# Kernel optimization log

Hardware: AMD Instinct MI355X
Metric: run time of the kernel (lower is better)

The kernel has to match this reference:

```python
import jax, jax.numpy as jnp
import numpy as np

N = 100000   # nodes
E = 800000   # edges
F_IN, H, C = 128, 128, 47
L = 3        # layers


def setup_inputs() -> dict:
    key = jax.random.key(0)
    ks = jax.random.split(key, 10)
    x = jax.random.normal(ks[0], (N, F_IN), dtype=jnp.float32)
    src = jax.random.randint(ks[1], (E,), 0, N, dtype=jnp.int32)
    dst = jax.random.randint(ks[2], (E,), 0, N, dtype=jnp.int32)
    w = jax.random.uniform(ks[3], (L, E), dtype=jnp.float32)
    W0 = jax.random.normal(ks[4], (F_IN, H), dtype=jnp.float32) * 0.05
    b0 = jnp.zeros((H,), jnp.float32)
    W1 = jax.random.normal(ks[5], (H, H), dtype=jnp.float32) * 0.05
    b1 = jnp.zeros((H,), jnp.float32)
    W2 = jax.random.normal(ks[6], (H, C), dtype=jnp.float32) * 0.05
    b2 = jnp.zeros((C,), jnp.float32)
    return {"x": x, "src": src, "dst": dst, "w": w,
            "W0": W0, "b0": b0, "W1": W1, "b1": b1, "W2": W2, "b2": b2}


def reference(x, src, dst, w, W0, b0, W1, b1, W2, b2):
    seg = lambda v, idx: jax.ops.segment_sum(v, idx, num_segments=N)
    ones = jnp.ones((src.shape[0],), x.dtype)
    # DGL GraphConv norm='both': structural degrees, clamped to >= 1
    inv_sqrt_out = jnp.maximum(seg(ones, src), 1.0) ** -0.5  # [N]
    inv_sqrt_in = jnp.maximum(seg(ones, dst), 1.0) ** -0.5   # [N]

    def gcn_layer(h, we, W, b):
        h = h * inv_sqrt_out[:, None]          # src normalization
        h = h @ W                               # linear (commutes with linear agg)
        m = h[src] * we[:, None]                # edge-weighted messages [E, d]
        agg = seg(m, dst)                       # scatter-add to dst [N, d]
        return agg * inv_sqrt_in[:, None] + b   # dst normalization + bias

    h = jax.nn.relu(gcn_layer(x, w[0], W0, b0))
    h = jax.nn.relu(gcn_layer(h, w[1], W1, b1))
    return gcn_layer(h, w[2], W2, b2)
```

## Files before the change

kernel.cpp:

```cpp
#include <hip/hip_runtime.h>


typedef short s16x8 __attribute__((ext_vector_type(8)));
typedef float f32x4 __attribute__((ext_vector_type(4)));

static constexpr int CAP = 24;

__device__ __forceinline__ unsigned short f2bf(float f) {
    unsigned int u = __float_as_uint(f);
    u += 0x7FFFu + ((u >> 16) & 1u);
    return (unsigned short)(u >> 16);
}
__device__ __forceinline__ float bf2f(unsigned short v) {
    return __uint_as_float((unsigned int)v << 16);
}

__global__ __launch_bounds__(256)
void fill_bucket(const int* __restrict__ src, const int* __restrict__ dst,
                 const float* __restrict__ w, int E,
                 int* __restrict__ dego, int* __restrict__ cursor,
                 float4* __restrict__ swb,
                 int* __restrict__ spill_cnt, int2* __restrict__ spill) {
    int e = blockIdx.x * blockDim.x + threadIdx.x;
    if (e >= E) return;
    int s = src[e];
    int d = dst[e];
    atomicAdd(&dego[s], 1);
    int pos = atomicAdd(&cursor[d], 1);
    if (pos < CAP) {
        swb[(size_t)d * CAP + pos] =
            make_float4(__int_as_float(s), w[e], w[E + e], w[2 * (size_t)E + e]);
    } else {
        int sp = atomicAdd(spill_cnt, 1);
        spill[sp] = make_int2(d, e);
    }
}

__global__ void invsqrt_kernel(const int* __restrict__ dego, const int* __restrict__ degi,
                               float* __restrict__ invo, float* __restrict__ invi, int N) {
    int i = blockIdx.x * blockDim.x + threadIdx.x;
    if (i < N) {
        int a = dego[i]; if (a < 1) a = 1;
        int b = degi[i]; if (b < 1) b = 1;
        invo[i] = 1.0f / sqrtf((float)a);
        invi[i] = 1.0f / sqrtf((float)b);
    }
}

__global__ void pack_w(const float* __restrict__ W, int dact, int PC,
                       unsigned short* __restrict__ Wp) {
    int idx = blockIdx.x * blockDim.x + threadIdx.x;
    if (idx >= 128 * PC) return;
    int k = idx / PC, col = idx % PC;
    float v = (col < dact) ? W[(size_t)k * dact + col] : 0.0f;
    int CT = PC / 16;
    int kk = k >> 5, kr = k & 31;
    int lane = ((kr >> 3) << 4) | (col & 15);
    int ct = col >> 4, j = kr & 7;
    Wp[(((size_t)(kk * CT) + ct) * 64 + lane) * 8 + j] = f2bf(v);
}

__global__ __launch_bounds__(256)
void prescale(const float* __restrict__ x, const float* __restrict__ invo,
              unsigned short* __restrict__ xb, int N) {
    int gid = blockIdx.x * blockDim.x + threadIdx.x;
    if (gid >= N * 32) return;
    int row = gid >> 5;
    float s = invo[row];
    float4 v = *(const float4*)&x[(size_t)gid * 4];
    ushort4 o;
    o.x = f2bf(v.x * s); o.y = f2bf(v.y * s);
    o.z = f2bf(v.z * s); o.w = f2bf(v.w * s);
    *(ushort4*)&xb[(size_t)gid * 4] = o;
}

template<int PC>
__global__ __launch_bounds__(256)
void gemm_direct(const unsigned short* __restrict__ h,
                 const unsigned short* __restrict__ Wp,
                 unsigned short* __restrict__ y, int N) {
    constexpr int CT = PC / 16;
    const int lane = threadIdx.x & 63;
    const int wid  = threadIdx.x >> 6;
    const int row0 = blockIdx.x * 64 + wid * 16;
    const int kgrp = lane >> 4;
    const int c    = lane & 15;

    int ar = row0 + c;
    if (ar > N - 1) ar = N - 1;
    const unsigned short* hrow = &h[(size_t)ar * 128 + kgrp * 8];

    f32x4 acc[CT];
    #pragma unroll
    for (int ct = 0; ct < CT; ++ct) acc[ct] = {0.f, 0.f, 0.f, 0.f};

    #pragma unroll
    for (int kk = 0; kk < 4; ++kk) {
        s16x8 af = *(const s16x8*)&hrow[kk * 32];
        #pragma unroll
        for (int ct = 0; ct < CT; ++ct) {
            s16x8 bf = *(const s16x8*)&Wp[((size_t)(kk * CT + ct) * 64 + lane) * 8];
            acc[ct] = __builtin_amdgcn_mfma_f32_16x16x32_bf16(af, bf, acc[ct], 0, 0, 0);
        }
    }

    #pragma unroll
    for (int ct = 0; ct < CT; ++ct) {
        #pragma unroll
        for (int i = 0; i < 4; ++i) {
            int row = row0 + kgrp * 4 + i;
            if (row < N) y[(size_t)row * PC + ct * 16 + c] = f2bf(acc[ct][i]);
        }
    }
}

template<int PC, int WSEL, bool FINAL>
__global__ __launch_bounds__(256)
void gather_w(const unsigned short* __restrict__ yb, const float4* __restrict__ swb,
              const int* __restrict__ degi, const int* __restrict__ spill_cnt,
              const int2* __restrict__ spill, const int* __restrict__ src,
              const float* __restrict__ wl, const float* __restrict__ invi,
              const float* __restrict__ invo, const float* __restrict__ b,
              void* __restrict__ outp, int N) {
    constexpr int TPN = PC / 4;
    constexpr int EPG = 64 / TPN;
    const int n = blockIdx.x * 4 + (threadIdx.x >> 6);
    if (n >= N) return;
    const int t    = threadIdx.x & 63;
    const int lane = t & (TPN - 1);
    const int g    = t / TPN;

    const ushort4* yv = (const ushort4*)yb;
    const float4* rec = swb + (size_t)n * CAP;
    const int dg  = degi[n];
    const int cnt = dg < CAP ? dg : CAP;

    float a0 = 0.f, a1 = 0.f, a2 = 0.f, a3 = 0.f;
    int p = g;
    for (; p + EPG < cnt; p += 2 * EPG) {
        float4 m0 = rec[p];
        float4 m1 = rec[p + EPG];
        float w0 = (WSEL == 0) ? m0.y : (WSEL == 1) ? m0.z : m0.w;
        float w1 = (WSEL == 0) ? m1.y : (WSEL == 1) ? m1.z : m1.w;
        ushort4 v0 = yv[(size_t)__float_as_int(m0.x) * TPN + lane];
        ushort4 v1 = yv[(size_t)__float_as_int(m1.x) * TPN + lane];
        a0 = fmaf(bf2f(v0.x), w0, a0);
        a1 = fmaf(bf2f(v0.y), w0, a1);
        a2 = fmaf(bf2f(v0.z), w0, a2);
        a3 = fmaf(bf2f(v0.w), w0, a3);
        a0 = fmaf(bf2f(v1.x), w1, a0);
        a1 = fmaf(bf2f(v1.y), w1, a1);
        a2 = fmaf(bf2f(v1.z), w1, a2);
        a3 = fmaf(bf2f(v1.w), w1, a3);
    }
    if (p < cnt) {
        float4 m0 = rec[p];
        float w0 = (WSEL == 0) ? m0.y : (WSEL == 1) ? m0.z : m0.w;
        ushort4 v0 = yv[(size_t)__float_as_int(m0.x) * TPN + lane];
        a0 = fmaf(bf2f(v0.x), w0, a0);
        a1 = fmaf(bf2f(v0.y), w0, a1);
        a2 = fmaf(bf2f(v0.z), w0, a2);
        a3 = fmaf(bf2f(v0.w), w0, a3);
    }
    if (dg > CAP && g == 0) {
        int sc = *spill_cnt;
        for (int i = 0; i < sc; ++i) {
            int2 sp = spill[i];
            if (sp.x == n) {
                int e = sp.y;
                int s0 = src[e];
                float w0 = wl[e];
                ushort4 v0 = yv[(size_t)s0 * TPN + lane];
                a0 = fmaf(bf2f(v0.x), w0, a0);
                a1 = fmaf(bf2f(v0.y), w0, a1);
                a2 = fmaf(bf2f(v0.z), w0, a2);
                a3 = fmaf(bf2f(v0.w), w0, a3);
            }
        }
    }

    #pragma unroll
    for (int m = TPN; m < 64; m <<= 1) {
        a0 += __shfl_xor(a0, m, 64);
        a1 += __shfl_xor(a1, m, 64);
        a2 += __shfl_xor(a2, m, 64);
        a3 += __shfl_xor(a3, m, 64);
    }
    if (g != 0) return;

    const float inv = invi[n];
    if (FINAL) {
        float* out = (float*)outp;
        const int c = lane * 4;
        float aa[4] = {a0, a1, a2, a3};
        #pragma unroll
        for (int j = 0; j < 4; ++j) {
            if (c + j < 47) out[(size_t)n * 47 + c + j] = fmaf(aa[j], inv, b[c + j]);
        }
    } else {
        unsigned short* out = (unsigned short*)outp;
        const float io = invo[n];
        float4 bb = *(const float4*)&b[lane * 4];
        float4 v;
        v.x = fmaxf(fmaf(a0, inv, bb.x), 0.f) * io;
        v.y = fmaxf(fmaf(a1, inv, bb.y), 0.f) * io;
        v.z = fmaxf(fmaf(a2, inv, bb.z), 0.f) * io;
        v.w = fmaxf(fmaf(a3, inv, bb.w), 0.f) * io;
        ushort4 o;
        o.x = f2bf(v.x); o.y = f2bf(v.y); o.z = f2bf(v.z); o.w = f2bf(v.w);
        *(ushort4*)&out[(size_t)n * PC + lane * 4] = o;
    }
}

extern "C" void kernel_launch(void* const* d_in, const int* in_sizes, int n_in,
                              void* d_out, int out_size, void* d_ws, size_t ws_size,
                              hipStream_t stream) {
    const float* x   = (const float*)d_in[0];
    const int*   src = (const int*)d_in[1];
    const int*   dst = (const int*)d_in[2];
    const float* w   = (const float*)d_in[3];
    const float* W0  = (const float*)d_in[4];
    const float* b0  = (const float*)d_in[5];
    const float* W1  = (const float*)d_in[6];
    const float* b1  = (const float*)d_in[7];
    const float* W2  = (const float*)d_in[8];
    const float* b2  = (const float*)d_in[9];

    const int N = in_sizes[0] / 128;
    const int E = in_sizes[1];

    char* p = (char*)d_ws;
    unsigned short* xh = (unsigned short*)p; p += (size_t)N * 128 * sizeof(unsigned short);
    unsigned short* y  = (unsigned short*)p; p += (size_t)N * 128 * sizeof(unsigned short);
    float4* swb    = (float4*)p; p += (size_t)N * CAP * sizeof(float4);
    int2*   spill  = (int2*)p;   p += (size_t)E * sizeof(int2);
    unsigned short* Wp = (unsigned short*)p; p += (size_t)(16384 * 2 + 8192) * sizeof(unsigned short);
    int*   dego    = (int*)p;    p += (size_t)N * sizeof(int);
    int*   cursor  = (int*)p;    p += (size_t)N * sizeof(int);
    int*   spill_cnt = (int*)p;  p += 4 * sizeof(int);
    float* invo    = (float*)p;  p += (size_t)N * sizeof(float);
    float* invi    = (float*)p;  p += (size_t)N * sizeof(float);

    unsigned short* Wp0 = Wp;
    unsigned short* Wp1 = Wp + 16384;
    unsigned short* Wp2 = Wp + 32768;

    pack_w<<<(128 * 128 + 255) / 256, 256, 0, stream>>>(W0, 128, 128, Wp0);
    pack_w<<<(128 * 128 + 255) / 256, 256, 0, stream>>>(W1, 128, 128, Wp1);
    pack_w<<<(128 * 64 + 255) / 256, 256, 0, stream>>>(W2, 47, 64, Wp2);

    hipMemsetAsync(dego, 0, (2 * (size_t)N + 4) * sizeof(int), stream);
    fill_bucket<<<(E + 255) / 256, 256, 0, stream>>>(
        src, dst, w, E, dego, cursor, swb, spill_cnt, spill);
    invsqrt_kernel<<<(N + 255) / 256, 256, 0, stream>>>(dego, cursor, invo, invi, N);

    prescale<<<(N * 32 + 255) / 256, 256, 0, stream>>>(x, invo, xh, N);

    const int gemm_blocks   = (N + 63) / 64;
    const int gather_blocks = (N + 3) / 4;

    gemm_direct<128><<<gemm_blocks, 256, 0, stream>>>(xh, Wp0, y, N);
    gather_w<128, 0, false><<<gather_blocks, 256, 0, stream>>>(
        y, swb, cursor, spill_cnt, spill, src, w, invi, invo, b0, xh, N);

    gemm_direct<128><<<gemm_blocks, 256, 0, stream>>>(xh, Wp1, y, N);
    gather_w<128, 1, false><<<gather_blocks, 256, 0, stream>>>(
        y, swb, cursor, spill_cnt, spill, src, w + E, invi, invo, b1, xh, N);

    gemm_direct<64><<<gemm_blocks, 256, 0, stream>>>(xh, Wp2, y, N);
    gather_w<64, 2, true><<<gather_blocks, 256, 0, stream>>>(
        y, swb, cursor, spill_cnt, spill, src, w + 2 * (size_t)E, invi, invo, b2, d_out, N);
}
```

Baseline: 294.6 us.

## Fuse edge bucketing with first GEMM and move src normalization into gather

Combines the three weight-pack kernels into one launch. Merges edge bucketing and the layer-0 GEMM into a single interleaved grid, where every third block runs the GEMM straight from fp32 x. Because the GEMM is linear, the source-degree scaling no longer has to happen before it: the gather loads dego[src] per edge and applies rsqrt itself. This removes the prescale, invsqrt and separate GEMM0 kernels and unrolls the gather loop by four. The cost is an extra random dego load and rsqrt per edge in every layer, and the GEMM blocks share the GPU with atomic-heavy fill blocks.

```diff
diff --git a/kernel.cpp b/kernel.cpp
--- a/kernel.cpp
+++ b/kernel.cpp
@@ -16,62 +16,95 @@
 }
 
 __global__ __launch_bounds__(256)
-void fill_bucket(const int* __restrict__ src, const int* __restrict__ dst,
-                 const float* __restrict__ w, int E,
-                 int* __restrict__ dego, int* __restrict__ cursor,
-                 float4* __restrict__ swb,
-                 int* __restrict__ spill_cnt, int2* __restrict__ spill) {
-    int e = blockIdx.x * blockDim.x + threadIdx.x;
-    if (e >= E) return;
-    int s = src[e];
-    int d = dst[e];
-    atomicAdd(&dego[s], 1);
-    int pos = atomicAdd(&cursor[d], 1);
-    if (pos < CAP) {
-        swb[(size_t)d * CAP + pos] =
-            make_float4(__int_as_float(s), w[e], w[E + e], w[2 * (size_t)E + e]);
+void pack_all(const float* __restrict__ W0, const float* __restrict__ W1,
+              const float* __restrict__ W2, unsigned short* __restrict__ Wp) {
+    int idx = blockIdx.x * 256 + threadIdx.x;
+    if (idx < 32768) {
+        const float* W = (idx < 16384) ? W0 : W1;
+        unsigned short* D = Wp + ((idx < 16384) ? 0 : 16384);
+        int i = idx & 16383;
+        int k = i >> 7, col = i & 127;
+        float v = W[k * 128 + col];
+        int kk = k >> 5, kr = k & 31;
+        int lane = ((kr >> 3) << 4) | (col & 15);
+        int ct = col >> 4, j = kr & 7;
+        D[(((kk * 8) + ct) * 64 + lane) * 8 + j] = f2bf(v);
+    } else if (idx < 40960) {
+        int i = idx - 32768;
+        int k = i >> 6, col = i & 63;
+        float v = (col < 47) ? W2[k * 47 + col] : 0.0f;
+        int kk = k >> 5, kr = k & 31;
+        int lane = ((kr >> 3) << 4) | (col & 15);
+        int ct = col >> 4, j = kr & 7;
+        (Wp + 32768)[(((kk * 4) + ct) * 64 + lane) * 8 + j] = f2bf(v);
+    }
+}
+
+__global__ __launch_bounds__(256)
+void mega_fill_gemm0(const int* __restrict__ src, const int* __restrict__ dst,
+                     const float* __restrict__ w, int E,
+                     int* __restrict__ dego, int* __restrict__ cursor,
+                     float4* __restrict__ swb,
+                     int* __restrict__ spill_cnt, int2* __restrict__ spill,
+                     const float* __restrict__ x,
+                     const unsigned short* __restrict__ Wp0,
+                     unsigned short* __restrict__ y, int N, int gemm_blocks) {
+    const int b = blockIdx.x;
+    if (b % 3 == 2) {
+        const int gb = b / 3;
+        if (gb >= gemm_blocks) return;
+        const int lane = threadIdx.x & 63;
+        const int wid  = threadIdx.x >> 6;
+        const int row0 = gb * 64 + wid * 16;
+        const int kgrp = lane >> 4;
+        const int c    = lane & 15;
+        int ar = row0 + c;
+        if (ar > N - 1) ar = N - 1;
+        const float* xrow = &x[(size_t)ar * 128];
+
+        f32x4 acc[8];
+        #pragma unroll
+        for (int ct = 0; ct < 8; ++ct) acc[ct] = {0.f, 0.f, 0.f, 0.f};
+
+        #pragma unroll
+        for (int kk = 0; kk < 4; ++kk) {
+            float4 u0 = *(const float4*)&xrow[kk * 32 + kgrp * 8];
+            float4 u1 = *(const float4*)&xrow[kk * 32 + kgrp * 8 + 4];
+            s16x8 af;
+            af[0] = (short)f2bf(u0.x); af[1] = (short)f2bf(u0.y);
+            af[2] = (short)f2bf(u0.z); af[3] = (short)f2bf(u0.w);
+            af[4] = (short)f2bf(u1.x); af[5] = (short)f2bf(u1.y);
+            af[6] = (short)f2bf(u1.z); af[7] = (short)f2bf(u1.w);
+            #pragma unroll
+            for (int ct = 0; ct < 8; ++ct) {
+                s16x8 bf = *(const s16x8*)&Wp0[((size_t)(kk * 8 + ct) * 64 + lane) * 8];
+                acc[ct] = __builtin_amdgcn_mfma_f32_16x16x32_bf16(af, bf, acc[ct], 0, 0, 0);
+            }
+        }
+        #pragma unroll
+        for (int ct = 0; ct < 8; ++ct) {
+            #pragma unroll
+            for (int i = 0; i < 4; ++i) {
+                int row = row0 + kgrp * 4 + i;
+                if (row < N) y[(size_t)row * 128 + ct * 16 + c] = f2bf(acc[ct][i]);
+            }
+        }
     } else {
-        int sp = atomicAdd(spill_cnt, 1);
-        spill[sp] = make_int2(d, e);
-    }
-}
-
-__global__ void invsqrt_kernel(const int* __restrict__ dego, const int* __restrict__ degi,
-                               float* __restrict__ invo, float* __restrict__ invi, int N) {
-    int i = blockIdx.x * blockDim.x + threadIdx.x;
-    if (i < N) {
-        int a = dego[i]; if (a < 1) a = 1;
-        int b = degi[i]; if (b < 1) b = 1;
-        invo[i] = 1.0f / sqrtf((float)a);
-        invi[i] = 1.0f / sqrtf((float)b);
-    }
-}
-
-__global__ void pack_w(const float* __restrict__ W, int dact, int PC,
-                       unsigned short* __restrict__ Wp) {
-    int idx = blockIdx.x * blockDim.x + threadIdx.x;
-    if (idx >= 128 * PC) return;
-    int k = idx / PC, col = idx % PC;
-    float v = (col < dact) ? W[(size_t)k * dact + col] : 0.0f;
-    int CT = PC / 16;
-    int kk = k >> 5, kr = k & 31;
-    int lane = ((kr >> 3) << 4) | (col & 15);
-    int ct = col >> 4, j = kr & 7;
-    Wp[(((size_t)(kk * CT) + ct) * 64 + lane) * 8 + j] = f2bf(v);
-}
-
-__global__ __launch_bounds__(256)
-void prescale(const float* __restrict__ x, const float* __restrict__ invo,
-              unsigned short* __restrict__ xb, int N) {
-    int gid = blockIdx.x * blockDim.x + threadIdx.x;
-    if (gid >= N * 32) return;
-    int row = gid >> 5;
-    float s = invo[row];
-    float4 v = *(const float4*)&x[(size_t)gid * 4];
-    ushort4 o;
-    o.x = f2bf(v.x * s); o.y = f2bf(v.y * s);
-    o.z = f2bf(v.z * s); o.w = f2bf(v.w * s);
-    *(ushort4*)&xb[(size_t)gid * 4] = o;
+        const int fb = b - b / 3;
+        int e = fb * 256 + (int)threadIdx.x;
+        if (e >= E) return;
+        int s = src[e];
+        int d = dst[e];
+        atomicAdd(&dego[s], 1);
+        int pos = atomicAdd(&cursor[d], 1);
+        if (pos < CAP) {
+            swb[(size_t)d * CAP + pos] =
+                make_float4(__int_as_float(s), w[e], w[E + e], w[2 * (size_t)E + e]);
+        } else {
+            int sp = atomicAdd(spill_cnt, 1);
+            spill[sp] = make_int2(d, e);
+        }
+    }
 }
 
 template<int PC>
@@ -117,11 +150,10 @@
 template<int PC, int WSEL, bool FINAL>
 __global__ __launch_bounds__(256)
 void gather_w(const unsigned short* __restrict__ yb, const float4* __restrict__ swb,
-              const int* __restrict__ degi, const int* __restrict__ spill_cnt,
-              const int2* __restrict__ spill, const int* __restrict__ src,
-              const float* __restrict__ wl, const float* __restrict__ invi,
-              const float* __restrict__ invo, const float* __restrict__ b,
-              void* __restrict__ outp, int N) {
+              const int* __restrict__ degi, const int* __restrict__ dego,
+              const int* __restrict__ spill_cnt, const int2* __restrict__ spill,
+              const int* __restrict__ src, const float* __restrict__ wl,
+              const float* __restrict__ b, void* __restrict__ outp, int N) {
     constexpr int TPN = PC / 4;
     constexpr int EPG = 64 / TPN;
     const int n = blockIdx.x * 4 + (threadIdx.x >> 6);
@@ -137,30 +169,40 @@
 
     float a0 = 0.f, a1 = 0.f, a2 = 0.f, a3 = 0.f;
     int p = g;
+
+#define SELW(m) ((WSEL == 0) ? (m).y : (WSEL == 1) ? (m).z : (m).w)
+#define EDGE_FMA(m, v) do {                                                   \
+        int _s = __float_as_int((m).x);                                       \
+        int _d = dego[_s]; if (_d < 1) _d = 1;                                \
+        float _w = SELW(m) * rsqrtf((float)_d);                               \
+        a0 = fmaf(bf2f((v).x), _w, a0);                                       \
+        a1 = fmaf(bf2f((v).y), _w, a1);                                       \
+        a2 = fmaf(bf2f((v).z), _w, a2);                                       \
+        a3 = fmaf(bf2f((v).w), _w, a3);                                       \
+    } while (0)
+
+    for (; p + 3 * EPG < cnt; p += 4 * EPG) {
+        float4 m0 = rec[p];
+        float4 m1 = rec[p + EPG];
+        float4 m2 = rec[p + 2 * EPG];
+        float4 m3 = rec[p + 3 * EPG];
+        ushort4 v0 = yv[(size_t)__float_as_int(m0.x) * TPN + lane];
+        ushort4 v1 = yv[(size_t)__float_as_int(m1.x) * TPN + lane];
+        ushort4 v2 = yv[(size_t)__float_as_int(m2.x) * TPN + lane];
+        ushort4 v3 = yv[(size_t)__float_as_int(m3.x) * TPN + lane];
+        EDGE_FMA(m0, v0); EDGE_FMA(m1, v1); EDGE_FMA(m2, v2); EDGE_FMA(m3, v3);
+    }
     for (; p + EPG < cnt; p += 2 * EPG) {
         float4 m0 = rec[p];
         float4 m1 = rec[p + EPG];
-        float w0 = (WSEL == 0) ? m0.y : (WSEL == 1) ? m0.z : m0.w;
-        float w1 = (WSEL == 0) ? m1.y : (WSEL == 1) ? m1.z : m1.w;
         ushort4 v0 = yv[(size_t)__float_as_int(m0.x) * TPN + lane];
         ushort4 v1 = yv[(size_t)__float_as_int(m1.x) * TPN + lane];
-        a0 = fmaf(bf2f(v0.x), w0, a0);
-        a1 = fmaf(bf2f(v0.y), w0, a1);
-        a2 = fmaf(bf2f(v0.z), w0, a2);
-        a3 = fmaf(bf2f(v0.w), w0, a3);
-        a0 = fmaf(bf2f(v1.x), w1, a0);
-        a1 = fmaf(bf2f(v1.y), w1, a1);
-        a2 = fmaf(bf2f(v1.z), w1, a2);
-        a3 = fmaf(bf2f(v1.w), w1, a3);
+        EDGE_FMA(m0, v0); EDGE_FMA(m1, v1);
     }
     if (p < cnt) {
         float4 m0 = rec[p];
-        float w0 = (WSEL == 0) ? m0.y : (WSEL == 1) ? m0.z : m0.w;
         ushort4 v0 = yv[(size_t)__float_as_int(m0.x) * TPN + lane];
-        a0 = fmaf(bf2f(v0.x), w0, a0);
-        a1 = fmaf(bf2f(v0.y), w0, a1);
-        a2 = fmaf(bf2f(v0.z), w0, a2);
-        a3 = fmaf(bf2f(v0.w), w0, a3);
+        EDGE_FMA(m0, v0);
     }
     if (dg > CAP && g == 0) {
         int sc = *spill_cnt;
@@ -169,7 +211,8 @@
             if (sp.x == n) {
                 int e = sp.y;
                 int s0 = src[e];
-                float w0 = wl[e];
+                int d0 = dego[s0]; if (d0 < 1) d0 = 1;
+                float w0 = wl[e] * rsqrtf((float)d0);
                 ushort4 v0 = yv[(size_t)s0 * TPN + lane];
                 a0 = fmaf(bf2f(v0.x), w0, a0);
                 a1 = fmaf(bf2f(v0.y), w0, a1);
@@ -178,6 +221,8 @@
             }
         }
     }
+#undef EDGE_FMA
+#undef SELW
 
     #pragma unroll
     for (int m = TPN; m < 64; m <<= 1) {
@@ -188,7 +233,7 @@
     }
     if (g != 0) return;
 
-    const float inv = invi[n];
+    const float inv = rsqrtf((float)(dg < 1 ? 1 : dg));
     if (FINAL) {
         float* out = (float*)outp;
         const int c = lane * 4;
@@ -199,13 +244,12 @@
         }
     } else {
         unsigned short* out = (unsigned short*)outp;
-        const float io = invo[n];
         float4 bb = *(const float4*)&b[lane * 4];
         float4 v;
-        v.x = fmaxf(fmaf(a0, inv, bb.x), 0.f) * io;
-        v.y = fmaxf(fmaf(a1, inv, bb.y), 0.f) * io;
-        v.z = fmaxf(fmaf(a2, inv, bb.z), 0.f) * io;
-        v.w = fmaxf(fmaf(a3, inv, bb.w), 0.f) * io;
+        v.x = fmaxf(fmaf(a0, inv, bb.x), 0.f);
+        v.y = fmaxf(fmaf(a1, inv, bb.y), 0.f);
+        v.z = fmaxf(fmaf(a2, inv, bb.z), 0.f);
+        v.w = fmaxf(fmaf(a3, inv, bb.w), 0.f);
         ushort4 o;
         o.x = f2bf(v.x); o.y = f2bf(v.y); o.z = f2bf(v.z); o.w = f2bf(v.w);
         *(ushort4*)&out[(size_t)n * PC + lane * 4] = o;
@@ -238,36 +282,31 @@
     int*   dego    = (int*)p;    p += (size_t)N * sizeof(int);
     int*   cursor  = (int*)p;    p += (size_t)N * sizeof(int);
     int*   spill_cnt = (int*)p;  p += 4 * sizeof(int);
-    float* invo    = (float*)p;  p += (size_t)N * sizeof(float);
-    float* invi    = (float*)p;  p += (size_t)N * sizeof(float);
-
-    unsigned short* Wp0 = Wp;
+
     unsigned short* Wp1 = Wp + 16384;
     unsigned short* Wp2 = Wp + 32768;
 
-    pack_w<<<(128 * 128 + 255) / 256, 256, 0, stream>>>(W0, 128, 128, Wp0);
-    pack_w<<<(128 * 128 + 255) / 256, 256, 0, stream>>>(W1, 128, 128, Wp1);
-    pack_w<<<(128 * 64 + 255) / 256, 256, 0, stream>>>(W2, 47, 64, Wp2);
-
     hipMemsetAsync(dego, 0, (2 * (size_t)N + 4) * sizeof(int), stream);
-    fill_bucket<<<(E + 255) / 256, 256, 0, stream>>>(
-        src, dst, w, E, dego, cursor, swb, spill_cnt, spill);
-    invsqrt_kernel<<<(N + 255) / 256, 256, 0, stream>>>(dego, cursor, invo, invi, N);
-
-    prescale<<<(N * 32 + 255) / 256, 256, 0, stream>>>(x, invo, xh, N);
-
-    const int gemm_blocks   = (N + 63) / 64;
+    pack_all<<<160, 256, 0, stream>>>(W0, W1, W2, Wp);
+
+    const int gemm_blocks = (N + 63) / 64;
+    const int fill_blocks = (E + 255) / 256;
+    int grid = 3 * gemm_blocks;
+    if (grid - grid / 3 < fill_blocks) grid = (3 * fill_blocks + 1) / 2 + 2;
+    mega_fill_gemm0<<<grid, 256, 0, stream>>>(
+        src, dst, w, E, dego, cursor, swb, spill_cnt, spill,
+        x, Wp, y, N, gemm_blocks);
+
     const int gather_blocks = (N + 3) / 4;
 
-    gemm_direct<128><<<gemm_blocks, 256, 0, stream>>>(xh, Wp0, y, N);
     gather_w<128, 0, false><<<gather_blocks, 256, 0, stream>>>(
-        y, swb, cursor, spill_cnt, spill, src, w, invi, invo, b0, xh, N);
+        y, swb, cursor, dego, spill_cnt, spill, src, w, b0, xh, N);
 
     gemm_direct<128><<<gemm_blocks, 256, 0, stream>>>(xh, Wp1, y, N);
     gather_w<128, 1, false><<<gather_blocks, 256, 0, stream>>>(
-        y, swb, cursor, spill_cnt, spill, src, w + E, invi, invo, b1, xh, N);
+        y, swb, cursor, dego, spill_cnt, spill, src, w + E, b1, xh, N);
 
     gemm_direct<64><<<gemm_blocks, 256, 0, stream>>>(xh, Wp2, y, N);
     gather_w<64, 2, true><<<gather_blocks, 256, 0, stream>>>(
-        y, swb, cursor, spill_cnt, spill, src, w + 2 * (size_t)E, invi, invo, b2, d_out, N);
-}
+        y, swb, cursor, dego, spill_cnt, spill, src, w + 2 * (size_t)E, b2, d_out, N);
+}
```

Result: faster. 255.0 us (-13.4%).
